# Performance work log

Measured on AMD Instinct MI355X. Metric: run time of the kernel, lower is better.

Reference implementation:

```python
import jax, jax.numpy as jnp
import numpy as np

VOCAB = 32000
NUM_CLASS = 16
HID = 256
BATCH = 2048  # c dim
NSTEP = 1     # n dim


def setup_inputs() -> dict:
    key = jax.random.key(0)
    ks = jax.random.split(key, 8)
    x = jax.random.randint(ks[0], (BATCH,), 0, VOCAB)
    z = jax.random.randint(ks[1], (NSTEP, BATCH), 0, NUM_CLASS)
    h = jax.random.normal(ks[2], (BATCH, NSTEP, HID), dtype=jnp.float32)
    E = jax.random.normal(ks[3], (VOCAB, HID), dtype=jnp.float32) * 0.02
    Vw = jax.random.normal(ks[4], (VOCAB, HID), dtype=jnp.float32) * 0.02
    Vb = jnp.zeros((VOCAB,), dtype=jnp.float32)
    W = jax.random.normal(ks[5], (NUM_CLASS, HID, HID), dtype=jnp.float32) * 0.02
    U = jax.random.normal(ks[6], (NUM_CLASS, HID, HID), dtype=jnp.float32) * 0.02
    return {"x": x, "z": z, "h": h, "E": E, "Vw": Vw, "Vb": Vb, "W": W, "U": U}


def reference(x, z, h, E, Vw, Vb, W, U):
    # e: (c, hid) embedding lookup
    e = E[x]
    # gather per-class weight banks: (n, c, k, h)
    Wz = W[z]
    Uz = U[z]
    # batched GEMV over gathered weights + tanh RNN step -> (n, c, k)
    h_t = jnp.tanh(
        jnp.einsum('nckh,ch->nck', Wz, e)
        + jnp.einsum('nckh,cnh->nck', Uz, h)
    ).transpose(1, 0, 2)  # (c, n, k)
    # output projection V: (c, n, vocab)
    logits = jnp.einsum('cnk,vk->cnv', h_t, Vw) + Vb
    return (logits, h_t)
```

## Files before the change

kernel.cpp:

```cpp
#include <hip/hip_runtime.h>
#include <hip/hip_bf16.h>

#define VOCAB 32000
#define NUM_CLASS 16
#define HID 256
#define KCAT 512
#define BATCH 2048

typedef __attribute__((ext_vector_type(8))) __bf16 bf16x8;
typedef __attribute__((ext_vector_type(4))) float floatx4;

__device__ __forceinline__ unsigned short f32_to_bf16_u16(float f) {
    union { float f; unsigned u; } a;
    a.f = f;
    unsigned r = a.u + 0x7fffu + ((a.u >> 16) & 1u);
    return (unsigned short)(r >> 16);
}

struct bf8v { unsigned short s[8]; };

__device__ __forceinline__ void lds_load16(unsigned short* lds, const unsigned short* g) {
    __builtin_amdgcn_global_load_lds(
        (const __attribute__((address_space(1))) unsigned int*)g,
        (__attribute__((address_space(3))) unsigned int*)lds, 16, 0, 0);
}

#define PREP_G   (BATCH * KCAT / 8)
#define PREP_WU  (NUM_CLASS * HID * KCAT / 8)
#define PREP_VW  (VOCAB * HID / 8)
#define PREP_TOT (PREP_G + PREP_WU + PREP_VW)
#define PREP_BLOCKS (PREP_TOT / 256)

__global__ __launch_bounds__(256) void prep_bucket_kernel(
    const int* __restrict__ x, const float* __restrict__ E,
    const float* __restrict__ h,
    const float* __restrict__ W, const float* __restrict__ U,
    const float* __restrict__ Vw, const int* __restrict__ z,
    unsigned short* __restrict__ G, unsigned short* __restrict__ Bcat,
    unsigned short* __restrict__ Vw_bf,
    int* __restrict__ perm, int* __restrict__ counts, int* __restrict__ bases)
{
    if (blockIdx.x == PREP_BLOCKS) {
        __shared__ int s_cnt[NUM_CLASS];
        __shared__ int s_off[NUM_CLASS];
        const int t = threadIdx.x;
        if (t < NUM_CLASS) s_cnt[t] = 0;
        __syncthreads();
        for (int c = t; c < BATCH; c += 256) atomicAdd(&s_cnt[z[c]], 1);
        __syncthreads();
        if (t == 0) {
            int acc = 0;
            for (int i = 0; i < NUM_CLASS; ++i) { s_off[i] = acc; acc += s_cnt[i]; }
        }
        __syncthreads();
        if (t < NUM_CLASS) { counts[t] = s_cnt[t]; bases[t] = s_off[t]; }
        __syncthreads();
        for (int c = t; c < BATCH; c += 256) {
            int p = atomicAdd(&s_off[z[c]], 1);
            perm[p] = c;
        }
        return;
    }

    const int tid = blockIdx.x * 256 + threadIdx.x;
    const float* src;
    unsigned short* dst;
    if (tid < PREP_G) {
        const int c  = tid >> 6;
        const int j0 = (tid & 63) * 8;
        src = (j0 < HID) ? (E + (size_t)x[c] * HID + j0)
                         : (h + (size_t)c * HID + (j0 - HID));
        dst = G + (size_t)c * KCAT + j0;
    } else if (tid < PREP_G + PREP_WU) {
        const int idx = tid - PREP_G;
        const int row = idx >> 6;
        const int j0  = (idx & 63) * 8;
        src = (j0 < HID) ? (W + (size_t)row * HID + j0)
                         : (U + (size_t)row * HID + (j0 - HID));
        dst = Bcat + (size_t)row * KCAT + j0;
    } else {
        const int idx = tid - (PREP_G + PREP_WU);
        src = Vw + (size_t)idx * 8;
        dst = Vw_bf + (size_t)idx * 8;
    }
    float4 v0 = ((const float4*)src)[0];
    float4 v1 = ((const float4*)src)[1];
    bf8v o;
    o.s[0] = f32_to_bf16_u16(v0.x); o.s[1] = f32_to_bf16_u16(v0.y);
    o.s[2] = f32_to_bf16_u16(v0.z); o.s[3] = f32_to_bf16_u16(v0.w);
    o.s[4] = f32_to_bf16_u16(v1.x); o.s[5] = f32_to_bf16_u16(v1.y);
    o.s[6] = f32_to_bf16_u16(v1.z); o.s[7] = f32_to_bf16_u16(v1.w);
    *(bf8v*)dst = o;
}

__global__ __launch_bounds__(256) void rnn_gemm_kernel(
    const unsigned short* __restrict__ G,
    const unsigned short* __restrict__ Bcat,
    const int* __restrict__ perm, const int* __restrict__ counts,
    const int* __restrict__ bases,
    float* __restrict__ ht_f32, unsigned short* __restrict__ ht_bf16)
{
    const int g = blockIdx.y;
    const int cnt = counts[g];
    const int mstart = blockIdx.x * 32;
    if (mstart >= cnt) return;
    const int base = bases[g];

    __shared__ int s_rows[32];
    if (threadIdx.x < 32) {
        int mi = mstart + threadIdx.x;
        s_rows[threadIdx.x] = perm[base + (mi < cnt ? mi : cnt - 1)];
    }
    __syncthreads();

    const int lane = threadIdx.x & 63;
    const int wave = threadIdx.x >> 6;
    const int n0   = wave * 64;
    const int lrow = lane & 15;
    const int quad = lane >> 4;
    const int kq   = quad * 8;

    const unsigned short* Bg = Bcat + (size_t)g * HID * KCAT;

    floatx4 acc[2][4] = {};
#pragma unroll 4
    for (int k0 = 0; k0 < KCAT; k0 += 32) {
        bf16x8 a[2], b[4];
#pragma unroll
        for (int mi = 0; mi < 2; ++mi) {
            const int row = s_rows[mi * 16 + lrow];
            a[mi] = *(const bf16x8*)(G + (size_t)row * KCAT + k0 + kq);
        }
#pragma unroll
        for (int ni = 0; ni < 4; ++ni)
            b[ni] = *(const bf16x8*)(Bg + (size_t)(n0 + ni * 16 + lrow) * KCAT + k0 + kq);
#pragma unroll
        for (int mi = 0; mi < 2; ++mi)
#pragma unroll
            for (int ni = 0; ni < 4; ++ni)
                acc[mi][ni] = __builtin_amdgcn_mfma_f32_16x16x32_bf16(
                    a[mi], b[ni], acc[mi][ni], 0, 0, 0);
    }

#pragma unroll
    for (int mi = 0; mi < 2; ++mi) {
#pragma unroll
        for (int r = 0; r < 4; ++r) {
            const int midx = mi * 16 + quad * 4 + r;
            if (mstart + midx >= cnt) continue;
            const int c = s_rows[midx];
#pragma unroll
            for (int ni = 0; ni < 4; ++ni) {
                const int k = n0 + ni * 16 + lrow;
                const float v = tanhf(acc[mi][ni][r]);
                ht_f32 [(size_t)c * HID + k] = v;
                ht_bf16[(size_t)c * HID + k] = f32_to_bf16_u16(v);
            }
        }
    }
}

__global__ __launch_bounds__(256) void out_gemm_kernel(
    const unsigned short* __restrict__ A,
    const unsigned short* __restrict__ B,
    const float* __restrict__ Vb,
    float* __restrict__ C)
{
    __shared__ unsigned short sA[2][128 * 32];
    __shared__ unsigned short sB[2][128 * 32];

    const int id  = blockIdx.x;
    const int sid = (id & 7) * 500 + (id >> 3);
    const int n0  = (sid >> 4) * 128;
    const int m0  = (sid & 15) * 128;

    const int lane = threadIdx.x & 63;
    const int wave = threadIdx.x >> 6;
    const int wr = wave >> 1, wc = wave & 1;
    const int lrow = lane & 15;
    const int quad = lane >> 4;

    const int srow   = lane >> 2;
    const int schunk = (lane & 3) ^ ((lane >> 3) & 3);

    const int rslot = quad ^ ((lrow >> 1) & 3);

    floatx4 acc[4][4] = {};

#pragma unroll
    for (int it = 0; it < 2; ++it) {
        const int wl = wave * 2 + it;
        const int r  = wl * 16 + srow;
        lds_load16(&sA[0][wl * 512], A + (size_t)(m0 + r) * HID + schunk * 8);
        lds_load16(&sB[0][wl * 512], B + (size_t)(n0 + r) * HID + schunk * 8);
    }
    __syncthreads();

#pragma unroll
    for (int kt = 0; kt < 8; ++kt) {
        const int cur = kt & 1;
        if (kt < 7) {
            const int k0n = (kt + 1) * 32;
#pragma unroll
            for (int it = 0; it < 2; ++it) {
                const int wl = wave * 2 + it;
                const int r  = wl * 16 + srow;
                lds_load16(&sA[cur ^ 1][wl * 512],
                           A + (size_t)(m0 + r) * HID + k0n + schunk * 8);
                lds_load16(&sB[cur ^ 1][wl * 512],
                           B + (size_t)(n0 + r) * HID + k0n + schunk * 8);
            }
        }

        bf16x8 a[4], b[4];
#pragma unroll
        for (int mi = 0; mi < 4; ++mi) {
            const int ra = wr * 64 + mi * 16 + lrow;
            a[mi] = *(const bf16x8*)&sA[cur][ra * 32 + rslot * 8];
        }
#pragma unroll
        for (int ni = 0; ni < 4; ++ni) {
            const int rb = wc * 64 + ni * 16 + lrow;
            b[ni] = *(const bf16x8*)&sB[cur][rb * 32 + rslot * 8];
        }
#pragma unroll
        for (int mi = 0; mi < 4; ++mi)
#pragma unroll
            for (int ni = 0; ni < 4; ++ni)
                acc[mi][ni] = __builtin_amdgcn_mfma_f32_16x16x32_bf16(
                    a[mi], b[ni], acc[mi][ni], 0, 0, 0);

        __syncthreads();
    }

    const int m_wave = m0 + wr * 64;
    const int n_wave = n0 + wc * 64;
    const int row_q  = quad * 4;
#pragma unroll
    for (int ni = 0; ni < 4; ++ni) {
        const int col = n_wave + ni * 16 + lrow;
        const float vb = Vb[col];
#pragma unroll
        for (int mi = 0; mi < 4; ++mi) {
            float* cp = C + (size_t)(m_wave + mi * 16 + row_q) * VOCAB + col;
#pragma unroll
            for (int r = 0; r < 4; ++r)
                __builtin_nontemporal_store(acc[mi][ni][r] + vb, cp + (size_t)r * VOCAB);
        }
    }
}

extern "C" void kernel_launch(void* const* d_in, const int* in_sizes, int n_in,
                              void* d_out, int out_size, void* d_ws, size_t ws_size,
                              hipStream_t stream) {
    const int*   x  = (const int*)d_in[0];
    const int*   z  = (const int*)d_in[1];
    const float* h  = (const float*)d_in[2];
    const float* E  = (const float*)d_in[3];
    const float* Vw = (const float*)d_in[4];
    const float* Vb = (const float*)d_in[5];
    const float* W  = (const float*)d_in[6];
    const float* U  = (const float*)d_in[7];

    float* logits = (float*)d_out;
    float* ht_out = logits + (size_t)BATCH * VOCAB;

    char* p = (char*)d_ws;
    unsigned short* Vw_bf = (unsigned short*)p;  p += (size_t)VOCAB * HID * 2;
    unsigned short* ht_bf = (unsigned short*)p;  p += (size_t)BATCH * HID * 2;
    unsigned short* G     = (unsigned short*)p;  p += (size_t)BATCH * KCAT * 2;
    unsigned short* Bcat  = (unsigned short*)p;  p += (size_t)NUM_CLASS * HID * KCAT * 2;
    int* perm   = (int*)p;  p += BATCH * 4;
    int* counts = (int*)p;  p += NUM_CLASS * 4;
    int* bases  = (int*)p;  p += NUM_CLASS * 4;

    prep_bucket_kernel<<<PREP_BLOCKS + 1, 256, 0, stream>>>(
        x, E, h, W, U, Vw, z, G, Bcat, Vw_bf, perm, counts, bases);
    rnn_gemm_kernel<<<dim3(BATCH / 32, NUM_CLASS), 256, 0, stream>>>(
        G, Bcat, perm, counts, bases, ht_out, ht_bf);
    out_gemm_kernel<<<4000, 256, 0, stream>>>(ht_bf, Vw_bf, Vb, logits);
}
```

Before: 413.7 us.

## Fuse bf16 conversion of Vw and gathered inputs into GEMM loads

Removes the separate conversion of Vw and the gathered E/h concat buffer from the prep kernel. The RNN GEMM now loads fp32 embedding rows and hidden states directly and converts them to bf16 in registers. The output GEMM reads fp32 Vw, converts it while staging into swizzled LDS through registers, and replaces the async global-to-LDS loads. This eliminates intermediate buffer writes and reads but doubles the bytes fetched for the B operand and adds conversion ALU work inside the GEMM.

```diff
diff --git a/kernel.cpp b/kernel.cpp
--- a/kernel.cpp
+++ b/kernel.cpp
@@ -19,28 +19,31 @@
 
 struct bf8v { unsigned short s[8]; };
 
-__device__ __forceinline__ void lds_load16(unsigned short* lds, const unsigned short* g) {
-    __builtin_amdgcn_global_load_lds(
-        (const __attribute__((address_space(1))) unsigned int*)g,
-        (__attribute__((address_space(3))) unsigned int*)lds, 16, 0, 0);
-}
-
-#define PREP_G   (BATCH * KCAT / 8)
-#define PREP_WU  (NUM_CLASS * HID * KCAT / 8)
-#define PREP_VW  (VOCAB * HID / 8)
-#define PREP_TOT (PREP_G + PREP_WU + PREP_VW)
-#define PREP_BLOCKS (PREP_TOT / 256)
+__device__ __forceinline__ bf8v pack8(float4 u, float4 v) {
+    bf8v o;
+    o.s[0] = f32_to_bf16_u16(u.x); o.s[1] = f32_to_bf16_u16(u.y);
+    o.s[2] = f32_to_bf16_u16(u.z); o.s[3] = f32_to_bf16_u16(u.w);
+    o.s[4] = f32_to_bf16_u16(v.x); o.s[5] = f32_to_bf16_u16(v.y);
+    o.s[6] = f32_to_bf16_u16(v.z); o.s[7] = f32_to_bf16_u16(v.w);
+    return o;
+}
+
+__device__ __forceinline__ bf16x8 cvt8(float4 u, float4 v) {
+    bf8v o = pack8(u, v);
+    union { bf8v s; bf16x8 b; } c;
+    c.s = o;
+    return c.b;
+}
+
+#define PREP_WU_BLOCKS (NUM_CLASS * HID * KCAT / 8 / 256)
 
 __global__ __launch_bounds__(256) void prep_bucket_kernel(
-    const int* __restrict__ x, const float* __restrict__ E,
-    const float* __restrict__ h,
     const float* __restrict__ W, const float* __restrict__ U,
-    const float* __restrict__ Vw, const int* __restrict__ z,
-    unsigned short* __restrict__ G, unsigned short* __restrict__ Bcat,
-    unsigned short* __restrict__ Vw_bf,
+    const int* __restrict__ z,
+    unsigned short* __restrict__ Bcat,
     int* __restrict__ perm, int* __restrict__ counts, int* __restrict__ bases)
 {
-    if (blockIdx.x == PREP_BLOCKS) {
+    if (blockIdx.x == PREP_WU_BLOCKS) {
         __shared__ int s_cnt[NUM_CLASS];
         __shared__ int s_off[NUM_CLASS];
         const int t = threadIdx.x;
@@ -63,38 +66,18 @@
     }
 
     const int tid = blockIdx.x * 256 + threadIdx.x;
-    const float* src;
-    unsigned short* dst;
-    if (tid < PREP_G) {
-        const int c  = tid >> 6;
-        const int j0 = (tid & 63) * 8;
-        src = (j0 < HID) ? (E + (size_t)x[c] * HID + j0)
-                         : (h + (size_t)c * HID + (j0 - HID));
-        dst = G + (size_t)c * KCAT + j0;
-    } else if (tid < PREP_G + PREP_WU) {
-        const int idx = tid - PREP_G;
-        const int row = idx >> 6;
-        const int j0  = (idx & 63) * 8;
-        src = (j0 < HID) ? (W + (size_t)row * HID + j0)
-                         : (U + (size_t)row * HID + (j0 - HID));
-        dst = Bcat + (size_t)row * KCAT + j0;
-    } else {
-        const int idx = tid - (PREP_G + PREP_WU);
-        src = Vw + (size_t)idx * 8;
-        dst = Vw_bf + (size_t)idx * 8;
-    }
+    const int row = tid >> 6;
+    const int j0  = (tid & 63) * 8;
+    const float* src = (j0 < HID) ? (W + (size_t)row * HID + j0)
+                                  : (U + (size_t)row * HID + (j0 - HID));
     float4 v0 = ((const float4*)src)[0];
     float4 v1 = ((const float4*)src)[1];
-    bf8v o;
-    o.s[0] = f32_to_bf16_u16(v0.x); o.s[1] = f32_to_bf16_u16(v0.y);
-    o.s[2] = f32_to_bf16_u16(v0.z); o.s[3] = f32_to_bf16_u16(v0.w);
-    o.s[4] = f32_to_bf16_u16(v1.x); o.s[5] = f32_to_bf16_u16(v1.y);
-    o.s[6] = f32_to_bf16_u16(v1.z); o.s[7] = f32_to_bf16_u16(v1.w);
-    *(bf8v*)dst = o;
+    *(bf8v*)(Bcat + (size_t)row * KCAT + j0) = pack8(v0, v1);
 }
 
 __global__ __launch_bounds__(256) void rnn_gemm_kernel(
-    const unsigned short* __restrict__ G,
+    const int* __restrict__ x, const float* __restrict__ E,
+    const float* __restrict__ h,
     const unsigned short* __restrict__ Bcat,
     const int* __restrict__ perm, const int* __restrict__ counts,
     const int* __restrict__ bases,
@@ -107,9 +90,12 @@
     const int base = bases[g];
 
     __shared__ int s_rows[32];
+    __shared__ int s_x[32];
     if (threadIdx.x < 32) {
         int mi = mstart + threadIdx.x;
-        s_rows[threadIdx.x] = perm[base + (mi < cnt ? mi : cnt - 1)];
+        int row = perm[base + (mi < cnt ? mi : cnt - 1)];
+        s_rows[threadIdx.x] = row;
+        s_x[threadIdx.x] = x[row];
     }
     __syncthreads();
 
@@ -123,13 +109,32 @@
     const unsigned short* Bg = Bcat + (size_t)g * HID * KCAT;
 
     floatx4 acc[2][4] = {};
+
 #pragma unroll 4
-    for (int k0 = 0; k0 < KCAT; k0 += 32) {
+    for (int k0 = 0; k0 < 256; k0 += 32) {
         bf16x8 a[2], b[4];
 #pragma unroll
         for (int mi = 0; mi < 2; ++mi) {
-            const int row = s_rows[mi * 16 + lrow];
-            a[mi] = *(const bf16x8*)(G + (size_t)row * KCAT + k0 + kq);
+            const float* s = E + (size_t)s_x[mi * 16 + lrow] * HID + k0 + kq;
+            a[mi] = cvt8(((const float4*)s)[0], ((const float4*)s)[1]);
+        }
+#pragma unroll
+        for (int ni = 0; ni < 4; ++ni)
+            b[ni] = *(const bf16x8*)(Bg + (size_t)(n0 + ni * 16 + lrow) * KCAT + k0 + kq);
+#pragma unroll
+        for (int mi = 0; mi < 2; ++mi)
+#pragma unroll
+            for (int ni = 0; ni < 4; ++ni)
+                acc[mi][ni] = __builtin_amdgcn_mfma_f32_16x16x32_bf16(
+                    a[mi], b[ni], acc[mi][ni], 0, 0, 0);
+    }
+#pragma unroll 4
+    for (int k0 = 256; k0 < 512; k0 += 32) {
+        bf16x8 a[2], b[4];
+#pragma unroll
+        for (int mi = 0; mi < 2; ++mi) {
+            const float* s = h + (size_t)s_rows[mi * 16 + lrow] * HID + (k0 - 256) + kq;
+            a[mi] = cvt8(((const float4*)s)[0], ((const float4*)s)[1]);
         }
 #pragma unroll
         for (int ni = 0; ni < 4; ++ni)
@@ -162,7 +167,7 @@
 
 __global__ __launch_bounds__(256) void out_gemm_kernel(
     const unsigned short* __restrict__ A,
-    const unsigned short* __restrict__ B,
+    const float* __restrict__ Bf,
     const float* __restrict__ Vb,
     float* __restrict__ C)
 {
@@ -180,36 +185,42 @@
     const int lrow = lane & 15;
     const int quad = lane >> 4;
 
-    const int srow   = lane >> 2;
-    const int schunk = (lane & 3) ^ ((lane >> 3) & 3);
+    const int srow = threadIdx.x >> 1;
+    const int sc0  = (threadIdx.x & 1) * 2;
+    const int ss0  = (sc0    ) ^ ((srow >> 1) & 3);
+    const int ss1  = (sc0 + 1) ^ ((srow >> 1) & 3);
+    const unsigned short* asrc = A  + (size_t)(m0 + srow) * HID + sc0 * 8;
+    const float*          bsrc = Bf + (size_t)(n0 + srow) * HID + sc0 * 8;
 
     const int rslot = quad ^ ((lrow >> 1) & 3);
 
     floatx4 acc[4][4] = {};
 
-#pragma unroll
-    for (int it = 0; it < 2; ++it) {
-        const int wl = wave * 2 + it;
-        const int r  = wl * 16 + srow;
-        lds_load16(&sA[0][wl * 512], A + (size_t)(m0 + r) * HID + schunk * 8);
-        lds_load16(&sB[0][wl * 512], B + (size_t)(n0 + r) * HID + schunk * 8);
+    {
+        bf8v  a0 = ((const bf8v*)asrc)[0];
+        bf8v  a1 = ((const bf8v*)asrc)[1];
+        float4 w0 = ((const float4*)bsrc)[0], w1 = ((const float4*)bsrc)[1];
+        float4 w2 = ((const float4*)bsrc)[2], w3 = ((const float4*)bsrc)[3];
+        *(bf8v*)&sA[0][srow * 32 + ss0 * 8] = a0;
+        *(bf8v*)&sA[0][srow * 32 + ss1 * 8] = a1;
+        *(bf8v*)&sB[0][srow * 32 + ss0 * 8] = pack8(w0, w1);
+        *(bf8v*)&sB[0][srow * 32 + ss1 * 8] = pack8(w2, w3);
     }
     __syncthreads();
 
 #pragma unroll
     for (int kt = 0; kt < 8; ++kt) {
         const int cur = kt & 1;
+        bf8v a0, a1;
+        float4 w0, w1, w2, w3;
         if (kt < 7) {
             const int k0n = (kt + 1) * 32;
-#pragma unroll
-            for (int it = 0; it < 2; ++it) {
-                const int wl = wave * 2 + it;
-                const int r  = wl * 16 + srow;
-                lds_load16(&sA[cur ^ 1][wl * 512],
-                           A + (size_t)(m0 + r) * HID + k0n + schunk * 8);
-                lds_load16(&sB[cur ^ 1][wl * 512],
-                           B + (size_t)(n0 + r) * HID + k0n + schunk * 8);
-            }
+            const unsigned short* as = asrc + k0n;
+            const float*          bs = bsrc + k0n;
+            a0 = ((const bf8v*)as)[0];
+            a1 = ((const bf8v*)as)[1];
+            w0 = ((const float4*)bs)[0]; w1 = ((const float4*)bs)[1];
+            w2 = ((const float4*)bs)[2]; w3 = ((const float4*)bs)[3];
         }
 
         bf16x8 a[4], b[4];
@@ -230,6 +241,12 @@
                 acc[mi][ni] = __builtin_amdgcn_mfma_f32_16x16x32_bf16(
                     a[mi], b[ni], acc[mi][ni], 0, 0, 0);
 
+        if (kt < 7) {
+            *(bf8v*)&sA[cur ^ 1][srow * 32 + ss0 * 8] = a0;
+            *(bf8v*)&sA[cur ^ 1][srow * 32 + ss1 * 8] = a1;
+            *(bf8v*)&sB[cur ^ 1][srow * 32 + ss0 * 8] = pack8(w0, w1);
+            *(bf8v*)&sB[cur ^ 1][srow * 32 + ss1 * 8] = pack8(w2, w3);
+        }
         __syncthreads();
     }
 
@@ -266,17 +283,15 @@
     float* ht_out = logits + (size_t)BATCH * VOCAB;
 
     char* p = (char*)d_ws;
-    unsigned short* Vw_bf = (unsigned short*)p;  p += (size_t)VOCAB * HID * 2;
     unsigned short* ht_bf = (unsigned short*)p;  p += (size_t)BATCH * HID * 2;
-    unsigned short* G     = (unsigned short*)p;  p += (size_t)BATCH * KCAT * 2;
     unsigned short* Bcat  = (unsigned short*)p;  p += (size_t)NUM_CLASS * HID * KCAT * 2;
     int* perm   = (int*)p;  p += BATCH * 4;
     int* counts = (int*)p;  p += NUM_CLASS * 4;
     int* bases  = (int*)p;  p += NUM_CLASS * 4;
 
-    prep_bucket_kernel<<<PREP_BLOCKS + 1, 256, 0, stream>>>(
-        x, E, h, W, U, Vw, z, G, Bcat, Vw_bf, perm, counts, bases);
+    prep_bucket_kernel<<<PREP_WU_BLOCKS + 1, 256, 0, stream>>>(
+        W, U, z, Bcat, perm, counts, bases);
     rnn_gemm_kernel<<<dim3(BATCH / 32, NUM_CLASS), 256, 0, stream>>>(
-        G, Bcat, perm, counts, bases, ht_out, ht_bf);
-    out_gemm_kernel<<<4000, 256, 0, stream>>>(ht_bf, Vw_bf, Vb, logits);
-}
+        x, E, h, Bcat, perm, counts, bases, ht_out, ht_bf);
+    out_gemm_kernel<<<4000, 256, 0, stream>>>(ht_bf, Vw, Vb, logits);
+}
```

New measurement: 490.7 us. 18.6% more time.
